# Optimization experiments

Measured on AMD Instinct MI355X. Metric: run time of the kernel, lower is better.

## Reference

```python
import math
import jax, jax.numpy as jnp
import numpy as np

V = 256; PS = 4; D = 256; MAXR = 4; MINR = 2; WIN = 4; KRET = 8; LAMP = 0.2

def _ln(x, g, b):
    m = x.mean(-1, keepdims=True)
    v = ((x - m) ** 2).mean(-1, keepdims=True)
    return (x - m) / jnp.sqrt(v + 1e-5) * g + b

def _gelu(x):
    return jax.nn.gelu(x, approximate=False)  # torch nn.GELU default = exact erf

def setup_inputs():
    key = jax.random.key(0)
    ks = iter(jax.random.split(key, 64))
    def w(shape, s=0.02):
        return jax.random.normal(next(ks), shape, jnp.float32) * s
    B, T = 32, 2048
    x = jax.random.randint(next(ks), (B, T), 0, V)
    z = lambda *s: jnp.zeros(s, jnp.float32)
    o = lambda *s: jnp.ones(s, jnp.float32)
    return dict(
        x=x,
        emb=w((V, D)), pos=w((PS, D)),
        gru_wih=w((3 * D, D)), gru_whh=w((3 * D, D)), gru_bih=z(3 * D), gru_bhh=z(3 * D),
        pp_ln_g=o(D), pp_ln_b=z(D),
        sum_w=w((D, D)), sum_b=z(D),
        msg_w1=w((2 * D, D)), msg_b1=z(D), msg_w2=w((D, D)), msg_b2=z(D),
        upd_w1=w((2 * D, D)), upd_b1=z(D), upd_w2=w((D, D)), upd_b2=z(D),
        halt_w=w((D, 1)), halt_b=z(1),
        mp_ln_g=o(D), mp_ln_b=z(D),
        q_w=w((D, D)), q_b=z(D), k_w=w((D, D)), k_b=z(D),
        v_w=w((D, D)), v_b=z(D), o_w=w((D, D)), o_b=z(D),
        br_w=w((D, D)), br_b=z(D),
        f_ln_g=o(D), f_ln_b=z(D),
        head_w=w((D, V)),
    )

def _forward(x, emb, pos, gru_wih, gru_whh, gru_bih, gru_bhh, pp_ln_g, pp_ln_b,
             sum_w, sum_b, msg_w1, msg_b1, msg_w2, msg_b2, upd_w1, upd_b1,
             upd_w2, upd_b2, halt_w, halt_b, mp_ln_g, mp_ln_b,
             q_w, q_b, k_w, k_b, v_w, v_b, o_w, o_b, br_w, br_b,
             f_ln_g, f_ln_b, head_w):
    B, T = x.shape
    N = T // PS  # T chosen divisible by patch_size, so F.pad is a no-op
    patches = x.reshape(B * N, PS)
    # --- GRU patch processor (all patches processed identically -> batch them) ---
    hin = emb[patches] + pos[None, :, :]            # [BN, PS, D]
    xg = hin @ gru_wih.T + gru_bih                  # [BN, PS, 3D]
    def gru_step(hprev, xp):
        gh = hprev @ gru_whh.T + gru_bhh
        ir, iz, inn = jnp.split(xp, 3, axis=-1)
        hr, hz, hn = jnp.split(gh, 3, axis=-1)
        r = jax.nn.sigmoid(ir + hr)
        zg = jax.nn.sigmoid(iz + hz)
        n = jnp.tanh(inn + r * hn)
        h = (1 - zg) * n + zg * hprev
        return h, h
    h0 = jnp.zeros((B * N, D), xg.dtype)
    _, seq = jax.lax.scan(gru_step, h0, jnp.swapaxes(xg, 0, 1))
    local = _ln(jnp.swapaxes(seq, 0, 1), pp_ln_g, pp_ln_b).reshape(B, N, PS, D)
    summaries = local.mean(2) @ sum_w + sum_b       # [B, N, D]
    # --- local message passing with ACT halting (vectorized sliding window) ---
    idx = jnp.arange(N)[:, None] + jnp.arange(-WIN, 1)[None, :]
    valid = idx >= 0
    idxc = jnp.clip(idx, 0, N - 1)
    counts = valid.sum(1).astype(jnp.float32)                     # [N]
    h = summaries
    remaining = jnp.ones((B, N, 1), jnp.float32)
    output = jnp.zeros_like(h)
    kl = jnp.float32(0.0)
    for step in range(MAXR):
        nb = h[:, idxc]
        sr = jnp.broadcast_to(h[:, :, None, :], nb.shape)
        m = _gelu(jnp.concatenate([sr, nb], -1) @ msg_w1 + msg_b1) @ msg_w2 + msg_b2
        msgs = (m * valid[None, :, :, None]).sum(2) / counts[None, :, None]
        upd = _gelu(jnp.concatenate([h, msgs], -1) @ upd_w1 + upd_b1) @ upd_w2 + upd_b2
        h = _ln(h + upd, mp_ln_g, mp_ln_b)
        if step < MINR:
            hp = jnp.zeros((B, 1, 1), jnp.float32)
        elif step == MAXR - 1:
            hp = jnp.ones((B, 1, 1), jnp.float32)
        else:
            hp = jax.nn.sigmoid(h.mean(1, keepdims=True) @ halt_w + halt_b)  # [B,1,1]
        output = output + remaining * hp * h
        remaining = remaining * (1 - hp)
        p = LAMP * (1 - LAMP) ** step
        kl = kl + p * (math.log(p) - jnp.log(hp.mean() + 1e-8))
    kl = kl / MAXR
    # --- sparse top-k causal retrieval over patch summaries ---
    q = output @ q_w + q_b
    k = output @ k_w + k_b
    v = output @ v_w + v_b
    scores = jnp.einsum('bnd,bmd->bnm', q, k) / math.sqrt(D)
    causal = jnp.tril(jnp.ones((N, N), bool))
    scores = jnp.where(causal[None], scores, -jnp.inf)
    tv, ti = jax.lax.top_k(scores, KRET)
    bI = jnp.arange(B)[:, None, None]
    nI = jnp.arange(N)[None, :, None]
    sparse = jnp.full_like(scores, -jnp.inf).at[bI, nI, ti].set(tv)
    attn = jax.nn.softmax(sparse, axis=-1)
    retrieved = jnp.einsum('bnm,bmd->bnd', attn, v) @ o_w + o_b
    combined = output + retrieved
    broad = combined @ br_w + br_b                                # [B, N, D]
    final = (local + broad[:, :, None, :]).reshape(B, N * PS, D)
    logits = _ln(final, f_ln_g, f_ln_b) @ head_w                  # [B, T, V]
    return logits, kl

def reference(x, emb, pos, gru_wih, gru_whh, gru_bih, gru_bhh, pp_ln_g, pp_ln_b,
              sum_w, sum_b, msg_w1, msg_b1, msg_w2, msg_b2, upd_w1, upd_b1,
              upd_w2, upd_b2, halt_w, halt_b, mp_ln_g, mp_ln_b,
              q_w, q_b, k_w, k_b, v_w, v_b, o_w, o_b, br_w, br_b,
              f_ln_g, f_ln_b, head_w):
    return _forward(x, emb, pos, gru_wih, gru_whh, gru_bih, gru_bhh, pp_ln_g, pp_ln_b,
                    sum_w, sum_b, msg_w1, msg_b1, msg_w2, msg_b2, upd_w1, upd_b1,
                    upd_w2, upd_b2, halt_w, halt_b, mp_ln_g, mp_ln_b,
                    q_w, q_b, k_w, k_b, v_w, v_b, o_w, o_b, br_w, br_b,
                    f_ln_g, f_ln_b, head_w)
```

## Files before the change

kernel.cpp:

```cpp
#include <hip/hip_runtime.h>
#include <cmath>


constexpr int N_   = 512;
constexpr int B_   = 32;
constexpr int BN_  = B_ * N_;
constexpr int M1_  = BN_ * 4;

typedef short bf16x8 __attribute__((ext_vector_type(8)));
typedef float f32x4  __attribute__((ext_vector_type(4)));

__device__ __forceinline__ float gelu_f(float x) {
  return 0.5f * x * (1.0f + erff(x * 0.70710678118654752440f));
}
__device__ __forceinline__ float sigm_f(float x) {
  return 1.0f / (1.0f + expf(-x));
}
__device__ __forceinline__ unsigned short f2bf(float f) {
  union { float f; unsigned int u; } c; c.f = f;
  unsigned int u = c.u;
  u += 0x7FFFu + ((u >> 16) & 1u);
  return (unsigned short)(u >> 16);
}
__device__ __forceinline__ float bf2f(unsigned short u) {
  union { unsigned int u; float f; } c; c.u = ((unsigned int)u) << 16;
  return c.f;
}
__device__ __forceinline__ int phys(int g, int r) {
  return ((g << 6) | (r ^ g)) << 3;
}
__device__ __forceinline__ int phys128(int g, int r) {
  return ((g << 7) | (r ^ g)) << 3;
}
__device__ __forceinline__ int phys16(int g, int r) {
  return ((g << 4) | (r ^ g)) << 3;
}

template<int AMODE, int EPI, int COUT>
__global__ __launch_bounds__(256)
void gemm_big(const void* __restrict__ A, const unsigned short* __restrict__ Bt,
              const float* __restrict__ bias, void* __restrict__ C,
              int M, int Nn, int K, int bstride, int ldC)
{
  __shared__ short As[4 * 128 * 8];
  __shared__ short Bs[4 * 128 * 8];
  const int t  = threadIdx.x;
  const int m0 = blockIdx.y * 128, n0 = blockIdx.x * 128;
  const int lane = t & 63, w = t >> 6;
  const int wr = w >> 1, wc = w & 1;
  const int fr = lane & 15, fg = lane >> 4;

  f32x4 acc[4][4] = {};

  for (int k0 = 0; k0 < K; k0 += 32) {
    #pragma unroll
    for (int c = 0; c < 2; ++c) {
      int idx = t + c * 256;
      int row = idx >> 2, g = idx & 3;
      int kk = k0 + g * 8;
      bf16x8 av;
      if constexpr (AMODE == 1) {
        av = *(const bf16x8*)&((const unsigned short*)A)[(size_t)(m0 + row) * K + kk];
      } else {
        const float4* p = (const float4*)&((const float*)A)[(size_t)(m0 + row) * K + kk];
        float4 a = p[0], b = p[1];
        av[0]=(short)f2bf(a.x); av[1]=(short)f2bf(a.y); av[2]=(short)f2bf(a.z); av[3]=(short)f2bf(a.w);
        av[4]=(short)f2bf(b.x); av[5]=(short)f2bf(b.y); av[6]=(short)f2bf(b.z); av[7]=(short)f2bf(b.w);
      }
      *(bf16x8*)&As[phys128(g, row)] = av;
      *(bf16x8*)&Bs[phys128(g, row)] =
          *(const bf16x8*)&Bt[(size_t)(n0 + row) * bstride + kk];
    }
    __syncthreads();

    bf16x8 a[4], b[4];
    #pragma unroll
    for (int i = 0; i < 4; ++i)
      a[i] = *(const bf16x8*)&As[phys128(fg, wr * 64 + i * 16 + fr)];
    #pragma unroll
    for (int j = 0; j < 4; ++j)
      b[j] = *(const bf16x8*)&Bs[phys128(fg, wc * 64 + j * 16 + fr)];
    #pragma unroll
    for (int i = 0; i < 4; ++i)
      #pragma unroll
      for (int j = 0; j < 4; ++j)
        acc[i][j] = __builtin_amdgcn_mfma_f32_16x16x32_bf16(a[i], b[j], acc[i][j], 0, 0, 0);
    __syncthreads();
  }

  #pragma unroll
  for (int i = 0; i < 4; ++i)
    #pragma unroll
    for (int j = 0; j < 4; ++j) {
      int col = n0 + wc * 64 + j * 16 + fr;
      float bcol = bias ? bias[col] : 0.0f;
      #pragma unroll
      for (int r = 0; r < 4; ++r) {
        int row = m0 + wr * 64 + i * 16 + fg * 4 + r;
        float vv = acc[i][j][r] + bcol;
        if constexpr (EPI == 1) vv = gelu_f(vv);
        if constexpr (COUT == 0)
          ((float*)C)[(size_t)row * ldC + col] = vv;
        else
          ((unsigned short*)C)[(size_t)row * ldC + col] = f2bf(vv);
      }
    }
}

template<int MODE, int BSRC, int EPI, int COUT>
__global__ __launch_bounds__(256)
void gemm_mfma(const float* __restrict__ A, const void* __restrict__ Bsrc,
               const float* __restrict__ bias, void* __restrict__ C,
               int M, int Nn, int K, int bstride, int ldC,
               const float* __restrict__ P2,
               const float* __restrict__ emb, const float* __restrict__ pos)
{
  __shared__ short As[4 * 64 * 8];
  __shared__ short Bs[4 * 64 * 8];
  const int tid  = threadIdx.x;
  const int m0   = blockIdx.y * 64, n0 = blockIdx.x * 64;
  const int srow = tid >> 2, sg = tid & 3;
  const int lane = tid & 63, w = tid >> 6;
  const int wr   = w >> 1,  wc = w & 1;
  const int fr   = lane & 15, fg = lane >> 4;

  f32x4 acc[2][2] = {};

  for (int k0 = 0; k0 < K; k0 += 32) {
    {
      int m = m0 + srow, k = k0 + sg * 8;
      bf16x8 tv;
      if constexpr (MODE == 10) {
        if (k < 256)
          tv = *(const bf16x8*)&((const unsigned short*)A)[(size_t)m * 256 + k];
        else
          tv = *(const bf16x8*)&((const unsigned short*)P2)[(size_t)m * 256 + (k - 256)];
      } else if constexpr (MODE == 11) {
        if (k < 256) {
          const float4* p = (const float4*)(A + (size_t)m * 256 + k);
          float4 a = p[0], b = p[1];
          tv[0]=(short)f2bf(a.x); tv[1]=(short)f2bf(a.y); tv[2]=(short)f2bf(a.z); tv[3]=(short)f2bf(a.w);
          tv[4]=(short)f2bf(b.x); tv[5]=(short)f2bf(b.y); tv[6]=(short)f2bf(b.z); tv[7]=(short)f2bf(b.w);
        } else {
          tv = *(const bf16x8*)&((const unsigned short*)P2)[(size_t)m * 256 + (k - 256)];
        }
      } else {
        float v[8];
        if constexpr (MODE == 6) {
          const float* src = nullptr;
          if (m < 256) src = emb + (size_t)m * 256 + k;
          else if (m < 260) src = pos + (size_t)(m - 256) * 256 + k;
          if (src) {
            const float4* p = (const float4*)src;
            float4 a = p[0], b = p[1];
            v[0]=a.x; v[1]=a.y; v[2]=a.z; v[3]=a.w; v[4]=b.x; v[5]=b.y; v[6]=b.z; v[7]=b.w;
          } else {
            #pragma unroll
            for (int j = 0; j < 8; ++j) v[j] = 0.f;
          }
        } else if constexpr (MODE == 8) {
          #pragma unroll
          for (int j = 0; j < 8; ++j) v[j] = P2[(size_t)(k + j) * 256 + m];
        } else {
          const unsigned short* Ab = (const unsigned short*)A;
          const unsigned short* base = Ab + (size_t)m * 1024 + k;
          bf16x8 r0 = *(const bf16x8*)(base);
          bf16x8 r1 = *(const bf16x8*)(base + 256);
          bf16x8 r2 = *(const bf16x8*)(base + 512);
          bf16x8 r3 = *(const bf16x8*)(base + 768);
          #pragma unroll
          for (int j = 0; j < 8; ++j)
            v[j] = 0.25f * (bf2f((unsigned short)r0[j]) + bf2f((unsigned short)r1[j]) +
                            bf2f((unsigned short)r2[j]) + bf2f((unsigned short)r3[j]));
        }
        #pragma unroll
        for (int j = 0; j < 8; ++j) tv[j] = (short)f2bf(v[j]);
      }
      *(bf16x8*)&As[phys(sg, srow)] = tv;
    }
    if constexpr (BSRC == 0) {
      const unsigned short* Bt = (const unsigned short*)Bsrc;
      *(bf16x8*)&Bs[phys(sg, srow)] =
          *(const bf16x8*)&Bt[(size_t)(n0 + srow) * bstride + k0 + sg * 8];
    } else {
      const float* Bf = (const float*)Bsrc;
      const float4* p = (const float4*)(Bf + (size_t)(n0 + srow) * bstride + k0 + sg * 8);
      float4 a = p[0], b = p[1];
      bf16x8 tv;
      tv[0]=(short)f2bf(a.x); tv[1]=(short)f2bf(a.y); tv[2]=(short)f2bf(a.z); tv[3]=(short)f2bf(a.w);
      tv[4]=(short)f2bf(b.x); tv[5]=(short)f2bf(b.y); tv[6]=(short)f2bf(b.z); tv[7]=(short)f2bf(b.w);
      *(bf16x8*)&Bs[phys(sg, srow)] = tv;
    }
    __syncthreads();

    bf16x8 a0 = *(const bf16x8*)&As[phys(fg, wr * 32 + fr)];
    bf16x8 a1 = *(const bf16x8*)&As[phys(fg, wr * 32 + 16 + fr)];
    bf16x8 b0 = *(const bf16x8*)&Bs[phys(fg, wc * 32 + fr)];
    bf16x8 b1 = *(const bf16x8*)&Bs[phys(fg, wc * 32 + 16 + fr)];
    acc[0][0] = __builtin_amdgcn_mfma_f32_16x16x32_bf16(a0, b0, acc[0][0], 0, 0, 0);
    acc[0][1] = __builtin_amdgcn_mfma_f32_16x16x32_bf16(a0, b1, acc[0][1], 0, 0, 0);
    acc[1][0] = __builtin_amdgcn_mfma_f32_16x16x32_bf16(a1, b0, acc[1][0], 0, 0, 0);
    acc[1][1] = __builtin_amdgcn_mfma_f32_16x16x32_bf16(a1, b1, acc[1][1], 0, 0, 0);
    __syncthreads();
  }

  #pragma unroll
  for (int i = 0; i < 2; ++i) {
    #pragma unroll
    for (int j = 0; j < 2; ++j) {
      int row0 = m0 + wr * 32 + i * 16 + fg * 4;
      int col  = n0 + wc * 32 + j * 16 + fr;
      float bcol = bias ? bias[col] : 0.0f;
      #pragma unroll
      for (int r = 0; r < 4; ++r) {
        float vv = acc[i][j][r] + bcol;
        if constexpr (EPI == 1) vv = gelu_f(vv);
        int row = row0 + r;
        if constexpr (COUT == 0)
          ((float*)C)[(size_t)row * ldC + col] = vv;
        else
          ((unsigned short*)C)[(size_t)row * ldC + col] = f2bf(vv);
      }
    }
  }
}

template<int OUTM>
__global__ __launch_bounds__(256)
void gemm_ln(const unsigned short* __restrict__ U, const unsigned short* __restrict__ u2T,
             const float* __restrict__ bias, unsigned short* __restrict__ h,
             const float* __restrict__ g, const float* __restrict__ bb,
             const float* __restrict__ hp, float* __restrict__ outp)
{
  __shared__ short As[4 * 16 * 8];
  __shared__ short Bs[4 * 256 * 8];
  __shared__ float psum[4][16], pssq[4][16];
  const int m0 = blockIdx.x * 16;
  const int t  = threadIdx.x;
  const int lane = t & 63, w = t >> 6;
  const int fr = lane & 15, fg = lane >> 4;

  f32x4 acc[4] = {};
  for (int k0 = 0; k0 < 256; k0 += 32) {
    if (t < 64) {
      int row = t >> 2, gq = t & 3;
      *(bf16x8*)&As[phys16(gq, row)] =
          *(const bf16x8*)&U[(size_t)(m0 + row) * 256 + k0 + gq * 8];
    }
    const unsigned short* brow = u2T + (size_t)t * 256 + k0;
    #pragma unroll
    for (int gq = 0; gq < 4; ++gq)
      *(bf16x8*)&Bs[((gq << 8) | (t ^ gq)) << 3] = *(const bf16x8*)(brow + gq * 8);
    __syncthreads();
    bf16x8 a = *(const bf16x8*)&As[phys16(fg, fr)];
    #pragma unroll
    for (int j = 0; j < 4; ++j) {
      int n = 64 * w + 16 * j + fr;
      bf16x8 b = *(const bf16x8*)&Bs[((fg << 8) | (n ^ fg)) << 3];
      acc[j] = __builtin_amdgcn_mfma_f32_16x16x32_bf16(a, b, acc[j], 0, 0, 0);
    }
    __syncthreads();
  }

  float bcol[4], gv[4], bv[4];
  #pragma unroll
  for (int j = 0; j < 4; ++j) {
    int col = 64 * w + 16 * j + fr;
    bcol[j] = bias[col]; gv[j] = g[col]; bv[j] = bb[col];
  }
  float vsum[4] = {}, vssq[4] = {};
  #pragma unroll
  for (int j = 0; j < 4; ++j) {
    int col = 64 * w + 16 * j + fr;
    #pragma unroll
    for (int r = 0; r < 4; ++r) {
      int row = m0 + 4 * fg + r;
      float v = acc[j][r] + bcol[j] + bf2f(h[(size_t)row * 256 + col]);
      acc[j][r] = v;
      vsum[r] += v;
      vssq[r] += v * v;
    }
  }
  #pragma unroll
  for (int off = 1; off < 16; off <<= 1) {
    #pragma unroll
    for (int r = 0; r < 4; ++r) {
      vsum[r] += __shfl_xor(vsum[r], off, 64);
      vssq[r] += __shfl_xor(vssq[r], off, 64);
    }
  }
  if (fr == 0) {
    #pragma unroll
    for (int r = 0; r < 4; ++r) {
      psum[w][4 * fg + r] = vsum[r];
      pssq[w][4 * fg + r] = vssq[r];
    }
  }
  __syncthreads();

  float rem = 0.f;
  if constexpr (OUTM == 3) rem = 1.0f - hp[m0 >> 9];
  #pragma unroll
  for (int r = 0; r < 4; ++r) {
    int rr = 4 * fg + r;
    float s  = psum[0][rr] + psum[1][rr] + psum[2][rr] + psum[3][rr];
    float q2 = pssq[0][rr] + pssq[1][rr] + pssq[2][rr] + pssq[3][rr];
    float mean = s * (1.0f / 256.0f);
    float var  = q2 * (1.0f / 256.0f) - mean * mean;
    float inv  = rsqrtf(var + 1e-5f);
    int row = m0 + rr;
    #pragma unroll
    for (int j = 0; j < 4; ++j) {
      int col = 64 * w + 16 * j + fr;
      float y = (acc[j][r] - mean) * inv * gv[j] + bv[j];
      h[(size_t)row * 256 + col] = f2bf(y);
      if constexpr (OUTM == 3) outp[(size_t)row * 256 + col] += rem * y;
    }
  }
}

__global__ __launch_bounds__(256)
void scores_tri(const unsigned short* __restrict__ qkv, float* __restrict__ sc)
{
  int flat = blockIdx.x;
  int xcd = flat & 7, s = flat >> 3;
  int bhi = s / 36, tile = s - bhi * 36;
  int b = bhi * 8 + xcd;
  int ti = 0;
  while ((ti + 1) * (ti + 2) / 2 <= tile) ++ti;
  int tj = tile - ti * (ti + 1) / 2;
  const int m0 = ti * 64, n0 = tj * 64;
  const unsigned short* Aq = qkv + (size_t)b * N_ * 768;
  const unsigned short* Bk = Aq + 256;

  __shared__ short As[4 * 64 * 8];
  __shared__ short Bs[4 * 64 * 8];
  const int tid  = threadIdx.x;
  const int srow = tid >> 2, sg = tid & 3;
  const int lane = tid & 63, w = tid >> 6;
  const int wr   = w >> 1,  wc = w & 1;
  const int fr   = lane & 15, fg = lane >> 4;

  f32x4 acc[2][2] = {};
  for (int k0 = 0; k0 < 256; k0 += 32) {
    *(bf16x8*)&As[phys(sg, srow)] =
        *(const bf16x8*)&Aq[(size_t)(m0 + srow) * 768 + k0 + sg * 8];
    *(bf16x8*)&Bs[phys(sg, srow)] =
        *(const bf16x8*)&Bk[(size_t)(n0 + srow) * 768 + k0 + sg * 8];
    __syncthreads();
    bf16x8 a0 = *(const bf16x8*)&As[phys(fg, wr * 32 + fr)];
    bf16x8 a1 = *(const bf16x8*)&As[phys(fg, wr * 32 + 16 + fr)];
    bf16x8 b0 = *(const bf16x8*)&Bs[phys(fg, wc * 32 + fr)];
    bf16x8 b1 = *(const bf16x8*)&Bs[phys(fg, wc * 32 + 16 + fr)];
    acc[0][0] = __builtin_amdgcn_mfma_f32_16x16x32_bf16(a0, b0, acc[0][0], 0, 0, 0);
    acc[0][1] = __builtin_amdgcn_mfma_f32_16x16x32_bf16(a0, b1, acc[0][1], 0, 0, 0);
    acc[1][0] = __builtin_amdgcn_mfma_f32_16x16x32_bf16(a1, b0, acc[1][0], 0, 0, 0);
    acc[1][1] = __builtin_amdgcn_mfma_f32_16x16x32_bf16(a1, b1, acc[1][1], 0, 0, 0);
    __syncthreads();
  }
  float* scb = sc + (size_t)b * N_ * N_;
  #pragma unroll
  for (int i = 0; i < 2; ++i) {
    #pragma unroll
    for (int j = 0; j < 2; ++j) {
      int row0 = m0 + wr * 32 + i * 16 + fg * 4;
      int col  = n0 + wc * 32 + j * 16 + fr;
      #pragma unroll
      for (int r = 0; r < 4; ++r) {
        int row = row0 + r;
        float vv = acc[i][j][r] * 0.0625f;
        if (col > row) vv = -__builtin_inff();
        scb[(size_t)row * N_ + col] = vv;
      }
    }
  }
}

struct PrepJobs {
  const float* src[12];
  unsigned short* dst[12];
  int rows[12];
  int dstride[12];
  int strt[12];
};
__global__ __launch_bounds__(256)
void prep_w_k(PrepJobs pj)
{
  int jid = blockIdx.y;
  const float* src = pj.src[jid];
  unsigned short* dst = pj.dst[jid];
  int ds = pj.dstride[jid];
  int total = pj.rows[jid] << 8;
  if (pj.strt[jid]) {
    for (int i = blockIdx.x * 256 + threadIdx.x; i < total; i += gridDim.x * 256) {
      int k = i & 255, n = i >> 8;
      dst[(size_t)n * ds + k] = f2bf(src[i]);
    }
  } else {
    for (int i = blockIdx.x * 256 + threadIdx.x; i < total; i += gridDim.x * 256) {
      int k = i & 255, n = i >> 8;
      dst[(size_t)n * ds + k] = f2bf(src[(size_t)k * 256 + n]);
    }
  }
}

__global__ __launch_bounds__(256)
void biasprep_k(const float* __restrict__ upd_b1, const float* __restrict__ msg_b2,
                const float* __restrict__ upd_w1, const float* __restrict__ msg_b1,
                const float* __restrict__ o_b, const float* __restrict__ br_w,
                const float* __restrict__ br_b, const float* __restrict__ q_b,
                const float* __restrict__ k_b, const float* __restrict__ v_b,
                float* __restrict__ biasU, float* __restrict__ biasHsn,
                float* __restrict__ biasB2, float* __restrict__ bQKV)
{
  int c = threadIdx.x;
  float s = upd_b1[c];
  for (int k = 0; k < 256; ++k)
    s += msg_b2[k] * upd_w1[(size_t)(256 + k) * 256 + c];
  biasU[c] = s;
  biasHsn[c] = msg_b1[c];
  biasHsn[256 + c] = 0.f;
  float s2 = br_b[c];
  for (int k = 0; k < 256; ++k)
    s2 += o_b[k] * br_w[(size_t)k * 256 + c];
  biasB2[c] = s2;
  bQKV[c] = q_b[c]; bQKV[256 + c] = k_b[c]; bQKV[512 + c] = v_b[c];
}

template<int FIRST>
__global__ __launch_bounds__(256)
void gru_pw_k(const unsigned short* __restrict__ gh, const float* __restrict__ bhh,
              const float* __restrict__ embW, const int* __restrict__ x,
              const float* __restrict__ bih,
              float* __restrict__ h, unsigned short* __restrict__ local, int t)
{
  int i   = blockIdx.x * 256 + threadIdx.x;
  int row = i >> 8, d = i & 255;
  int tok = x[row * 4 + t];
  const float* er = embW + (size_t)tok * 768;
  const float* pr = embW + (size_t)(256 + t) * 768;
  float ir  = er[d]       + pr[d]       + bih[d];
  float iz  = er[256 + d] + pr[256 + d] + bih[256 + d];
  float inn = er[512 + d] + pr[512 + d] + bih[512 + d];
  float hr, hz, hn;
  if constexpr (FIRST) {
    hr = bhh[d]; hz = bhh[256 + d]; hn = bhh[512 + d];
  } else {
    const unsigned short* gr = gh + (size_t)row * 768;
    hr = bf2f(gr[d]); hz = bf2f(gr[256 + d]); hn = bf2f(gr[512 + d]);
  }
  float r  = sigm_f(ir + hr);
  float zg = sigm_f(iz + hz);
  float nn = tanhf(inn + r * hn);
  float hnew;
  if constexpr (FIRST) hnew = (1.0f - zg) * nn;
  else                 hnew = (1.0f - zg) * nn + zg * h[i];
  h[i] = hnew;
  local[((size_t)row * 4 + t) * 256 + d] = f2bf(hnew);
}

__global__ __launch_bounds__(256)
void smsg_k(const unsigned short* __restrict__ hsn, unsigned short* __restrict__ S)
{
  int i = blockIdx.x * 256 + threadIdx.x;
  int m = i >> 6, d4 = (i & 63) << 2;
  int n = m & (N_ - 1);
  ushort4 hsu = *(const ushort4*)&hsn[(size_t)m * 512 + d4];
  float hs0 = bf2f(hsu.x), hs1 = bf2f(hsu.y), hs2 = bf2f(hsu.z), hs3 = bf2f(hsu.w);
  float a0 = 0.f, a1 = 0.f, a2 = 0.f, a3 = 0.f;
  #pragma unroll
  for (int kk = 0; kk < 5; ++kk) {
    int idx = n + kk - 4;
    if (idx >= 0) {
      ushort4 hv = *(const ushort4*)&hsn[(size_t)(m + kk - 4) * 512 + 256 + d4];
      a0 += gelu_f(hs0 + bf2f(hv.x));
      a1 += gelu_f(hs1 + bf2f(hv.y));
      a2 += gelu_f(hs2 + bf2f(hv.z));
      a3 += gelu_f(hs3 + bf2f(hv.w));
    }
  }
  float sc1 = 1.0f / (float)((n < 4 ? n : 4) + 1);
  ushort4 o = {f2bf(a0 * sc1), f2bf(a1 * sc1), f2bf(a2 * sc1), f2bf(a3 * sc1)};
  *(ushort4*)&S[(size_t)m * 256 + d4] = o;
}

__global__ __launch_bounds__(256)
void ln_bf16_k(unsigned short* __restrict__ X, const float* __restrict__ g,
               const float* __restrict__ bb)
{
  int wave = threadIdx.x >> 6, lane = threadIdx.x & 63;
  int row  = blockIdx.x * 4 + wave;
  unsigned short* xr = X + (size_t)row * 256;
  ushort4 u = *(const ushort4*)&xr[lane * 4];
  float x[4] = {bf2f(u.x), bf2f(u.y), bf2f(u.z), bf2f(u.w)};
  float s = x[0] + x[1] + x[2] + x[3];
  #pragma unroll
  for (int off = 1; off < 64; off <<= 1) s += __shfl_xor(s, off, 64);
  float mean = s * (1.0f / 256.0f);
  float ss = 0.f;
  #pragma unroll
  for (int j = 0; j < 4; ++j) { float d = x[j] - mean; ss += d * d; }
  #pragma unroll
  for (int off = 1; off < 64; off <<= 1) ss += __shfl_xor(ss, off, 64);
  float inv = rsqrtf(ss * (1.0f / 256.0f) + 1e-5f);
  ushort4 o;
  o.x = f2bf((x[0] - mean) * inv * g[lane*4+0] + bb[lane*4+0]);
  o.y = f2bf((x[1] - mean) * inv * g[lane*4+1] + bb[lane*4+1]);
  o.z = f2bf((x[2] - mean) * inv * g[lane*4+2] + bb[lane*4+2]);
  o.w = f2bf((x[3] - mean) * inv * g[lane*4+3] + bb[lane*4+3]);
  *(ushort4*)&xr[lane * 4] = o;
}

__global__ __launch_bounds__(256)
void ln_cvt_k(const unsigned short* __restrict__ X, const float* __restrict__ Add,
              const float* __restrict__ g, const float* __restrict__ bb,
              unsigned short* __restrict__ Out)
{
  int wave = threadIdx.x >> 6, lane = threadIdx.x & 63;
  int row  = blockIdx.x * 4 + wave;
  ushort4 u = *(const ushort4*)&X[(size_t)row * 256 + lane * 4];
  const float4 ar = *(const float4*)&Add[(size_t)(row >> 2) * 256 + lane * 4];
  float x[4] = {bf2f(u.x) + ar.x, bf2f(u.y) + ar.y, bf2f(u.z) + ar.z, bf2f(u.w) + ar.w};
  float s = x[0] + x[1] + x[2] + x[3];
  #pragma unroll
  for (int off = 1; off < 64; off <<= 1) s += __shfl_xor(s, off, 64);
  float mean = s * (1.0f / 256.0f);
  float ss = 0.f;
  #pragma unroll
  for (int j = 0; j < 4; ++j) { float d = x[j] - mean; ss += d * d; }
  #pragma unroll
  for (int off = 1; off < 64; off <<= 1) ss += __shfl_xor(ss, off, 64);
  float inv = rsqrtf(ss * (1.0f / 256.0f) + 1e-5f);
  ushort4 o;
  o.x = f2bf((x[0] - mean) * inv * g[lane*4+0] + bb[lane*4+0]);
  o.y = f2bf((x[1] - mean) * inv * g[lane*4+1] + bb[lane*4+1]);
  o.z = f2bf((x[2] - mean) * inv * g[lane*4+2] + bb[lane*4+2]);
  o.w = f2bf((x[3] - mean) * inv * g[lane*4+3] + bb[lane*4+3]);
  *(ushort4*)&Out[(size_t)row * 256 + lane * 4] = o;
}

__global__ __launch_bounds__(256)
void halt1_k(const unsigned short* __restrict__ h, const float* __restrict__ hw,
             float* __restrict__ part)
{
  int b = blockIdx.x, s = blockIdx.y, tid = threadIdx.x;
  const unsigned short* p = h + ((size_t)b * N_ + s * 32) * 256;
  float acc = 0.f;
  for (int i = tid * 4; i < 32 * 256; i += 1024) {
    ushort4 u = *(const ushort4*)&p[i];
    const float4 w4 = *(const float4*)&hw[i & 255];
    acc += bf2f(u.x) * w4.x + bf2f(u.y) * w4.y + bf2f(u.z) * w4.z + bf2f(u.w) * w4.w;
  }
  __shared__ float red[256];
  red[tid] = acc; __syncthreads();
  for (int off = 128; off > 0; off >>= 1) {
    if (tid < off) red[tid] += red[tid + off];
    __syncthreads();
  }
  if (tid == 0) part[b * 16 + s] = red[0];
}
__global__ __launch_bounds__(64)
void halt2_k(const float* __restrict__ part, const float* __restrict__ hb,
             float* __restrict__ hp)
{
  int b = threadIdx.x;
  if (b < 32) {
    float s = 0.f;
    for (int i = 0; i < 16; ++i) s += part[b * 16 + i];
    hp[b] = sigm_f(s * (1.0f / (float)N_) + hb[0]);
  }
}
__global__ __launch_bounds__(256)
void out2_k(const unsigned short* __restrict__ h, const float* __restrict__ hp,
            float* __restrict__ outp)
{
  int i = blockIdx.x * 256 + threadIdx.x;
  outp[i] = hp[i >> 17] * bf2f(h[i]);
}

__global__ __launch_bounds__(256)
void topk_k(const float* __restrict__ sc, const unsigned short* __restrict__ qkv,
            unsigned short* __restrict__ rpre)
{
  const float NEG = -__builtin_inff();
  int wave = threadIdx.x >> 6, lane = threadIdx.x & 63;
  int rowg = blockIdx.x * 4 + wave;
  int b = rowg >> 9, n = rowg & (N_ - 1);
  const float* srow = sc + (size_t)rowg * N_;
  float v[8];
  #pragma unroll
  for (int j = 0; j < 8; ++j) {
    int col = lane + j * 64;
    v[j] = (col <= n) ? srow[col] : NEG;
  }
  float tv[8]; int ti[8];
  #pragma unroll
  for (int it = 0; it < 8; ++it) {
    float bv = v[0]; int bi = lane;
    #pragma unroll
    for (int j = 1; j < 8; ++j)
      if (v[j] > bv) { bv = v[j]; bi = lane + j * 64; }
    #pragma unroll
    for (int off = 1; off < 64; off <<= 1) {
      float ov = __shfl_xor(bv, off, 64);
      int   oi = __shfl_xor(bi, off, 64);
      if (ov > bv || (ov == bv && oi < bi)) { bv = ov; bi = oi; }
    }
    tv[it] = bv; ti[it] = bi;
    if ((bi & 63) == lane) v[bi >> 6] = NEG;
  }
  float mx = tv[0];
  float wsum = 0.f, wj[8];
  #pragma unroll
  for (int j = 0; j < 8; ++j) { wj[j] = expf(tv[j] - mx); wsum += wj[j]; }
  float inv = 1.0f / wsum;
  const unsigned short* vb = qkv + 512;
  int d0 = lane * 4;
  float a0 = 0.f, a1 = 0.f, a2 = 0.f, a3 = 0.f;
  #pragma unroll
  for (int j = 0; j < 8; ++j) {
    float wgt = wj[j] * inv;
    ushort4 vv = *(const ushort4*)&vb[((size_t)(b * N_ + ti[j])) * 768 + d0];
    a0 += wgt * bf2f(vv.x); a1 += wgt * bf2f(vv.y);
    a2 += wgt * bf2f(vv.z); a3 += wgt * bf2f(vv.w);
  }
  ushort4 o = {f2bf(a0), f2bf(a1), f2bf(a2), f2bf(a3)};
  *(ushort4*)&rpre[(size_t)rowg * 256 + d0] = o;
}

__global__ void kl_k(const float* __restrict__ hp, float* __restrict__ out)
{
  if (threadIdx.x == 0 && blockIdx.x == 0) {
    float hm = 0.f;
    for (int b = 0; b < 32; ++b) hm += hp[b];
    hm *= (1.0f / 32.0f);
    const float l1e8 = logf(1e-8f);
    float kl = 0.f;
    kl += 0.2f    * (logf(0.2f)    - l1e8);
    kl += 0.16f   * (logf(0.16f)   - l1e8);
    kl += 0.128f  * (logf(0.128f)  - logf(hm + 1e-8f));
    kl += 0.1024f * (logf(0.1024f) - logf(1.0f + 1e-8f));
    out[0] = kl * 0.25f;
  }
}

extern "C" void kernel_launch(void* const* d_in, const int* in_sizes, int n_in,
                              void* d_out, int out_size, void* d_ws, size_t ws_size,
                              hipStream_t stream)
{
  const int*   x       = (const int*)  d_in[0];
  const float* emb     = (const float*)d_in[1];
  const float* pos     = (const float*)d_in[2];
  const float* gru_wih = (const float*)d_in[3];
  const float* gru_whh = (const float*)d_in[4];
  const float* gru_bih = (const float*)d_in[5];
  const float* gru_bhh = (const float*)d_in[6];
  const float* pp_ln_g = (const float*)d_in[7];
  const float* pp_ln_b = (const float*)d_in[8];
  const float* sum_w   = (const float*)d_in[9];
  const float* sum_b   = (const float*)d_in[10];
  const float* msg_w1  = (const float*)d_in[11];
  const float* msg_b1  = (const float*)d_in[12];
  const float* msg_w2  = (const float*)d_in[13];
  const float* msg_b2  = (const float*)d_in[14];
  const float* upd_w1  = (const float*)d_in[15];
  const float* upd_b1  = (const float*)d_in[16];
  const float* upd_w2  = (const float*)d_in[17];
  const float* upd_b2  = (const float*)d_in[18];
  const float* halt_w  = (const float*)d_in[19];
  const float* halt_b  = (const float*)d_in[20];
  const float* mp_ln_g = (const float*)d_in[21];
  const float* mp_ln_b = (const float*)d_in[22];
  const float* q_w     = (const float*)d_in[23];
  const float* q_b     = (const float*)d_in[24];
  const float* k_w     = (const float*)d_in[25];
  const float* k_b     = (const float*)d_in[26];
  const float* v_w     = (const float*)d_in[27];
  const float* v_b     = (const float*)d_in[28];
  const float* o_w     = (const float*)d_in[29];
  const float* o_b     = (const float*)d_in[30];
  const float* br_w    = (const float*)d_in[31];
  const float* br_b    = (const float*)d_in[32];
  const float* f_ln_g  = (const float*)d_in[33];
  const float* f_ln_b  = (const float*)d_in[34];
  const float* head_w  = (const float*)d_in[35];

  constexpr size_t SZ_Q = (size_t)BN_ * 256;
  float* ws     = (float*)d_ws;
  float* R_h    = ws;
  float* R_outp = R_h    + SZ_Q;
  float* R_b1   = R_outp + SZ_Q;
  float* R_b2   = R_b1   + SZ_Q;
  float* R_b3   = R_b2   + SZ_Q;
  float* R_rp   = R_b3   + SZ_Q;
  unsigned short* R_loc = (unsigned short*)(R_rp + SZ_Q);
  unsigned short* wb = R_loc + 4 * SZ_Q;
  unsigned short* sumT  = wb;
  unsigned short* W1cT  = sumT  + 65536;
  unsigned short* u1cT  = W1cT  + 131072;
  unsigned short* u2T   = u1cT  + 131072;
  unsigned short* qkvT  = u2T   + 65536;
  unsigned short* brWT  = qkvT  + 196608;
  unsigned short* headT = brWT  + 131072;
  unsigned short* whhT  = headT + 65536;
  float* R_embW = (float*)(whhT + 196608);
  float* R_bU   = R_embW + 320 * 768;
  float* R_bH   = R_bU + 256;
  float* R_bB2  = R_bH + 512;
  float* R_bQKV = R_bB2 + 256;
  float* R_part = R_bQKV + 768;
  float* R_hp   = R_part + 512;

  unsigned short* R_hb = ((unsigned short*)R_b3) + SZ_Q;

  float* logits = (float*)d_out;
  dim3 blk(256);

  PrepJobs pj;
  const float* srcs[11] = {sum_w, msg_w1, msg_w1 + 65536, upd_w1, upd_w2,
                           q_w, k_w, v_w, br_w, head_w, gru_whh};
  unsigned short* dsts[11] = {sumT, W1cT, W1cT + 65536, u1cT, u2T,
                              qkvT, qkvT + 65536, qkvT + 131072, brWT, headT, whhT};
  int rows[11] = {256,256,256,256,256,256,256,256,256,256,768};
  int dstd[11] = {256,256,256,512,256,256,256,256,512,256,256};
  int strt[11] = {0,0,0,0,0,0,0,0,0,0,1};
  for (int i = 0; i < 11; ++i) {
    pj.src[i]=srcs[i]; pj.dst[i]=dsts[i]; pj.rows[i]=rows[i];
    pj.dstride[i]=dstd[i]; pj.strt[i]=strt[i];
  }
  prep_w_k<<<dim3(64, 11), blk, 0, stream>>>(pj);
  biasprep_k<<<dim3(1), blk, 0, stream>>>(upd_b1, msg_b2, upd_w1, msg_b1,
                                          o_b, br_w, br_b, q_b, k_b, v_b,
                                          R_bU, R_bH, R_bB2, R_bQKV);
  gemm_mfma<8, 1, 0, 1><<<dim3(4, 4), blk, 0, stream>>>(
      nullptr, msg_w2, nullptr, u1cT + 256, 256, 256, 256, 256, 512,
      upd_w1 + 65536, nullptr, nullptr);
  gemm_mfma<8, 1, 0, 1><<<dim3(4, 4), blk, 0, stream>>>(
      nullptr, o_w, nullptr, brWT + 256, 256, 256, 256, 256, 512,
      br_w, nullptr, nullptr);
  gemm_mfma<6, 1, 0, 0><<<dim3(12, 5), blk, 0, stream>>>(
      nullptr, gru_wih, nullptr, R_embW, 320, 768, 256, 256, 768,
      nullptr, emb, pos);

  unsigned short* ghB = (unsigned short*)R_b1;
  gru_pw_k<1><<<dim3(BN_), blk, 0, stream>>>(
      nullptr, gru_bhh, R_embW, x, gru_bih, R_h, R_loc, 0);
  for (int t = 1; t < 4; ++t) {
    gemm_big<0, 0, 1><<<dim3(6, 128), blk, 0, stream>>>(
        R_h, whhT, gru_bhh, ghB, BN_, 768, 256, 256, 768);
    gru_pw_k<0><<<dim3(BN_), blk, 0, stream>>>(
        ghB, gru_bhh, R_embW, x, gru_bih, R_h, R_loc, t);
  }
  ln_bf16_k<<<dim3(M1_ / 4), blk, 0, stream>>>(R_loc, pp_ln_g, pp_ln_b);

  gemm_mfma<9, 0, 0, 1><<<dim3(4, 256), blk, 0, stream>>>(
      (const float*)R_loc, sumT, sum_b, R_hb, BN_, 256, 256, 256, 256,
      nullptr, nullptr, nullptr);

  unsigned short* hsnB = (unsigned short*)R_b1;
  unsigned short* UB   = (unsigned short*)R_b2;
  unsigned short* Sb   = (unsigned short*)R_b3;
  for (int step = 0; step < 4; ++step) {
    gemm_big<1, 0, 1><<<dim3(4, 128), blk, 0, stream>>>(
        R_hb, W1cT, R_bH, hsnB, BN_, 512, 256, 256, 512);
    smsg_k<<<dim3(BN_ / 4), blk, 0, stream>>>(hsnB, Sb);
    gemm_mfma<10, 0, 1, 1><<<dim3(4, 256), blk, 0, stream>>>(
        (const float*)R_hb, u1cT, R_bU, UB, BN_, 256, 512, 512, 256,
        (const float*)Sb, nullptr, nullptr);
    if (step == 3) {
      gemm_ln<3><<<dim3(BN_ / 16), blk, 0, stream>>>(
          UB, u2T, upd_b2, R_hb, mp_ln_g, mp_ln_b, R_hp, R_outp);
    } else {
      gemm_ln<0><<<dim3(BN_ / 16), blk, 0, stream>>>(
          UB, u2T, upd_b2, R_hb, mp_ln_g, mp_ln_b, nullptr, nullptr);
      if (step == 2) {
        halt1_k<<<dim3(32, 16), blk, 0, stream>>>(R_hb, halt_w, R_part);
        halt2_k<<<dim3(1), dim3(64), 0, stream>>>(R_part, halt_b, R_hp);
        out2_k<<<dim3(BN_), blk, 0, stream>>>(R_hb, R_hp, R_outp);
      }
    }
  }

  unsigned short* qkv  = (unsigned short*)R_b3;
  unsigned short* rpre = ((unsigned short*)R_rp) + SZ_Q;
  float* sc = R_b1;
  gemm_big<0, 0, 1><<<dim3(6, 128), blk, 0, stream>>>(
      R_outp, qkvT, R_bQKV, qkv, BN_, 768, 256, 256, 768);
  scores_tri<<<dim3(1152), blk, 0, stream>>>(qkv, sc);
  topk_k<<<dim3(BN_ / 4), blk, 0, stream>>>(sc, qkv, rpre);

  float* broad = R_h;
  gemm_mfma<11, 0, 0, 0><<<dim3(4, 256), blk, 0, stream>>>(
      R_outp, brWT, R_bB2, broad, BN_, 256, 512, 512, 256,
      (const float*)rpre, nullptr, nullptr);

  unsigned short* Abuf = (unsigned short*)R_b1;
  ln_cvt_k<<<dim3(M1_ / 4), blk, 0, stream>>>(R_loc, broad, f_ln_g, f_ln_b, Abuf);
  gemm_big<1, 0, 0><<<dim3(2, 512), blk, 0, stream>>>(
      Abuf, headT, nullptr, logits, M1_, 256, 256, 256, 256);

  kl_k<<<dim3(1), dim3(64), 0, stream>>>(R_hp, logits + (size_t)M1_ * 256);
}
```

Measured before the change: 628.1 us.

## Fuse message aggregation, update MLP first layer, and LN GEMM into one kernel

Replaces the smsg_k kernel, the separate update-MLP first-layer GEMM and the gemm_ln kernel with a single msgtail_k per 16-row block. It computes the windowed GELU message sum into shared memory, runs the 512-wide first update GEMM with GELU into shared memory, then the second GEMM plus residual and LayerNorm. This removes two launches and the global round-trips of the S and U intermediates on each of the four message-passing steps. In exchange, each block now reloads the full u1cT weight matrix from global memory for only 16 rows, and the small per-block tile may reduce MFMA efficiency relative to the tiled GEMM it replaces.

```diff
diff --git a/kernel.cpp b/kernel.cpp
--- a/kernel.cpp
+++ b/kernel.cpp
@@ -32,8 +32,8 @@
 __device__ __forceinline__ int phys128(int g, int r) {
   return ((g << 7) | (r ^ g)) << 3;
 }
-__device__ __forceinline__ int phys16(int g, int r) {
-  return ((g << 4) | (r ^ g)) << 3;
+__device__ __forceinline__ int fidx(int kg, int r) {
+  return ((kg << 4) | (r ^ (kg & 3))) << 3;
 }
 
 template<int AMODE, int EPI, int COUT>
@@ -130,12 +130,7 @@
     {
       int m = m0 + srow, k = k0 + sg * 8;
       bf16x8 tv;
-      if constexpr (MODE == 10) {
-        if (k < 256)
-          tv = *(const bf16x8*)&((const unsigned short*)A)[(size_t)m * 256 + k];
-        else
-          tv = *(const bf16x8*)&((const unsigned short*)P2)[(size_t)m * 256 + (k - 256)];
-      } else if constexpr (MODE == 11) {
+      if constexpr (MODE == 11) {
         if (k < 256) {
           const float4* p = (const float4*)(A + (size_t)m * 256 + k);
           float4 a = p[0], b = p[1];
@@ -227,12 +222,18 @@
 
 template<int OUTM>
 __global__ __launch_bounds__(256)
-void gemm_ln(const unsigned short* __restrict__ U, const unsigned short* __restrict__ u2T,
-             const float* __restrict__ bias, unsigned short* __restrict__ h,
-             const float* __restrict__ g, const float* __restrict__ bb,
-             const float* __restrict__ hp, float* __restrict__ outp)
-{
-  __shared__ short As[4 * 16 * 8];
+void msgtail_k(const unsigned short* __restrict__ hsn,
+               const unsigned short* __restrict__ u1cT,
+               const unsigned short* __restrict__ u2T,
+               const float* __restrict__ biasU,
+               const float* __restrict__ ub2,
+               unsigned short* __restrict__ h,
+               const float* __restrict__ g, const float* __restrict__ bb,
+               const float* __restrict__ hp, float* __restrict__ outp)
+{
+  __shared__ short Hs[32 * 16 * 8];
+  __shared__ short Ss[32 * 16 * 8];
+  __shared__ short Us[32 * 16 * 8];
   __shared__ short Bs[4 * 256 * 8];
   __shared__ float psum[4][16], pssq[4][16];
   const int m0 = blockIdx.x * 16;
@@ -240,42 +241,98 @@
   const int lane = t & 63, w = t >> 6;
   const int fr = lane & 15, fg = lane >> 4;
 
-  f32x4 acc[4] = {};
-  for (int k0 = 0; k0 < 256; k0 += 32) {
-    if (t < 64) {
-      int row = t >> 2, gq = t & 3;
-      *(bf16x8*)&As[phys16(gq, row)] =
-          *(const bf16x8*)&U[(size_t)(m0 + row) * 256 + k0 + gq * 8];
-    }
-    const unsigned short* brow = u2T + (size_t)t * 256 + k0;
+  {
+    int r = t >> 4, c = t & 15;
+    int row = m0 + r;
+    int n = row & (N_ - 1);
+    float sc1 = 1.0f / (float)((n < 4 ? n : 4) + 1);
+    #pragma unroll
+    for (int half = 0; half < 2; ++half) {
+      int d0 = c * 16 + half * 8;
+      *(bf16x8*)&Hs[fidx(d0 >> 3, r)] =
+          *(const bf16x8*)&h[(size_t)row * 256 + d0];
+      bf16x8 hs = *(const bf16x8*)&hsn[(size_t)row * 512 + d0];
+      float acc[8] = {};
+      #pragma unroll
+      for (int kk = 0; kk < 5; ++kk) {
+        if (n + kk - 4 >= 0) {
+          bf16x8 hv = *(const bf16x8*)&hsn[(size_t)(row + kk - 4) * 512 + 256 + d0];
+          #pragma unroll
+          for (int e = 0; e < 8; ++e)
+            acc[e] += gelu_f(bf2f((unsigned short)hs[e]) + bf2f((unsigned short)hv[e]));
+        }
+      }
+      bf16x8 o;
+      #pragma unroll
+      for (int e = 0; e < 8; ++e) o[e] = (short)f2bf(acc[e] * sc1);
+      *(bf16x8*)&Ss[fidx(d0 >> 3, r)] = o;
+    }
+  }
+  __syncthreads();
+
+  f32x4 accU[4] = {};
+  for (int ks = 0; ks < 16; ++ks) {
+    const unsigned short* brow = u1cT + (size_t)t * 512 + ks * 32;
     #pragma unroll
     for (int gq = 0; gq < 4; ++gq)
       *(bf16x8*)&Bs[((gq << 8) | (t ^ gq)) << 3] = *(const bf16x8*)(brow + gq * 8);
     __syncthreads();
-    bf16x8 a = *(const bf16x8*)&As[phys16(fg, fr)];
+    int kg = ((ks & 7) << 2) | fg;
+    bf16x8 a = (ks < 8) ? *(const bf16x8*)&Hs[fidx(kg, fr)]
+                        : *(const bf16x8*)&Ss[fidx(kg, fr)];
     #pragma unroll
     for (int j = 0; j < 4; ++j) {
-      int n = 64 * w + 16 * j + fr;
-      bf16x8 b = *(const bf16x8*)&Bs[((fg << 8) | (n ^ fg)) << 3];
-      acc[j] = __builtin_amdgcn_mfma_f32_16x16x32_bf16(a, b, acc[j], 0, 0, 0);
-    }
-    __syncthreads();
-  }
-
-  float bcol[4], gv[4], bv[4];
+      int nn2 = 64 * w + 16 * j + fr;
+      bf16x8 b = *(const bf16x8*)&Bs[((fg << 8) | (nn2 ^ fg)) << 3];
+      accU[j] = __builtin_amdgcn_mfma_f32_16x16x32_bf16(a, b, accU[j], 0, 0, 0);
+    }
+    __syncthreads();
+  }
   #pragma unroll
   for (int j = 0; j < 4; ++j) {
     int col = 64 * w + 16 * j + fr;
-    bcol[j] = bias[col]; gv[j] = g[col]; bv[j] = bb[col];
-  }
-  float vsum[4] = {}, vssq[4] = {};
+    float bu = biasU[col];
+    #pragma unroll
+    for (int r = 0; r < 4; ++r) {
+      int rowl = 4 * fg + r;
+      Us[fidx(col >> 3, rowl) + (col & 7)] = (short)f2bf(gelu_f(accU[j][r] + bu));
+    }
+  }
+  __syncthreads();
+
+  f32x4 acc[4] = {};
+  for (int ks = 0; ks < 8; ++ks) {
+    const unsigned short* brow = u2T + (size_t)t * 256 + ks * 32;
+    #pragma unroll
+    for (int gq = 0; gq < 4; ++gq)
+      *(bf16x8*)&Bs[((gq << 8) | (t ^ gq)) << 3] = *(const bf16x8*)(brow + gq * 8);
+    __syncthreads();
+    int kg = (ks << 2) | fg;
+    bf16x8 a = *(const bf16x8*)&Us[fidx(kg, fr)];
+    #pragma unroll
+    for (int j = 0; j < 4; ++j) {
+      int nn2 = 64 * w + 16 * j + fr;
+      bf16x8 b = *(const bf16x8*)&Bs[((fg << 8) | (nn2 ^ fg)) << 3];
+      acc[j] = __builtin_amdgcn_mfma_f32_16x16x32_bf16(a, b, acc[j], 0, 0, 0);
+    }
+    __syncthreads();
+  }
+
+  float b2[4], gv[4], bv[4];
   #pragma unroll
   for (int j = 0; j < 4; ++j) {
     int col = 64 * w + 16 * j + fr;
+    b2[j] = ub2[col]; gv[j] = g[col]; bv[j] = bb[col];
+  }
+  float vsum[4] = {}, vssq[4] = {};
+  #pragma unroll
+  for (int j = 0; j < 4; ++j) {
+    int col = 64 * w + 16 * j + fr;
     #pragma unroll
     for (int r = 0; r < 4; ++r) {
-      int row = m0 + 4 * fg + r;
-      float v = acc[j][r] + bcol[j] + bf2f(h[(size_t)row * 256 + col]);
+      int rowl = 4 * fg + r;
+      float hv = bf2f((unsigned short)Hs[fidx(col >> 3, rowl) + (col & 7)]);
+      float v = acc[j][r] + b2[j] + hv;
       acc[j][r] = v;
       vsum[r] += v;
       vssq[r] += v * v;
@@ -457,31 +514,6 @@
   else                 hnew = (1.0f - zg) * nn + zg * h[i];
   h[i] = hnew;
   local[((size_t)row * 4 + t) * 256 + d] = f2bf(hnew);
-}
-
-__global__ __launch_bounds__(256)
-void smsg_k(const unsigned short* __restrict__ hsn, unsigned short* __restrict__ S)
-{
-  int i = blockIdx.x * 256 + threadIdx.x;
-  int m = i >> 6, d4 = (i & 63) << 2;
-  int n = m & (N_ - 1);
-  ushort4 hsu = *(const ushort4*)&hsn[(size_t)m * 512 + d4];
-  float hs0 = bf2f(hsu.x), hs1 = bf2f(hsu.y), hs2 = bf2f(hsu.z), hs3 = bf2f(hsu.w);
-  float a0 = 0.f, a1 = 0.f, a2 = 0.f, a3 = 0.f;
-  #pragma unroll
-  for (int kk = 0; kk < 5; ++kk) {
-    int idx = n + kk - 4;
-    if (idx >= 0) {
-      ushort4 hv = *(const ushort4*)&hsn[(size_t)(m + kk - 4) * 512 + 256 + d4];
-      a0 += gelu_f(hs0 + bf2f(hv.x));
-      a1 += gelu_f(hs1 + bf2f(hv.y));
-      a2 += gelu_f(hs2 + bf2f(hv.z));
-      a3 += gelu_f(hs3 + bf2f(hv.w));
-    }
-  }
-  float sc1 = 1.0f / (float)((n < 4 ? n : 4) + 1);
-  ushort4 o = {f2bf(a0 * sc1), f2bf(a1 * sc1), f2bf(a2 * sc1), f2bf(a3 * sc1)};
-  *(ushort4*)&S[(size_t)m * 256 + d4] = o;
 }
 
 __global__ __launch_bounds__(256)
@@ -758,21 +790,15 @@
       nullptr, nullptr, nullptr);
 
   unsigned short* hsnB = (unsigned short*)R_b1;
-  unsigned short* UB   = (unsigned short*)R_b2;
-  unsigned short* Sb   = (unsigned short*)R_b3;
   for (int step = 0; step < 4; ++step) {
     gemm_big<1, 0, 1><<<dim3(4, 128), blk, 0, stream>>>(
         R_hb, W1cT, R_bH, hsnB, BN_, 512, 256, 256, 512);
-    smsg_k<<<dim3(BN_ / 4), blk, 0, stream>>>(hsnB, Sb);
-    gemm_mfma<10, 0, 1, 1><<<dim3(4, 256), blk, 0, stream>>>(
-        (const float*)R_hb, u1cT, R_bU, UB, BN_, 256, 512, 512, 256,
-        (const float*)Sb, nullptr, nullptr);
     if (step == 3) {
-      gemm_ln<3><<<dim3(BN_ / 16), blk, 0, stream>>>(
-          UB, u2T, upd_b2, R_hb, mp_ln_g, mp_ln_b, R_hp, R_outp);
+      msgtail_k<3><<<dim3(BN_ / 16), blk, 0, stream>>>(
+          hsnB, u1cT, u2T, R_bU, upd_b2, R_hb, mp_ln_g, mp_ln_b, R_hp, R_outp);
     } else {
-      gemm_ln<0><<<dim3(BN_ / 16), blk, 0, stream>>>(
-          UB, u2T, upd_b2, R_hb, mp_ln_g, mp_ln_b, nullptr, nullptr);
+      msgtail_k<0><<<dim3(BN_ / 16), blk, 0, stream>>>(
+          hsnB, u1cT, u2T, R_bU, upd_b2, R_hb, mp_ln_g, mp_ln_b, nullptr, nullptr);
       if (step == 2) {
         halt1_k<<<dim3(32, 16), blk, 0, stream>>>(R_hb, halt_w, R_part);
         halt2_k<<<dim3(1), dim3(64), 0, stream>>>(R_part, halt_b, R_hp);
```

New measurement: 834.4 us. +32.8%, slower.
